# Kernel tuning notes

Measured on AMD Instinct MI355X. Metric: run time of the kernel, lower is better.

## Reference

```python
import jax, jax.numpy as jnp
import numpy as np

B, N1, N2, D, O = 4, 256, 256, 64, 64
TEMP = 1.0
BN_EPS = 1e-5


def setup_inputs() -> dict:
    key = jax.random.key(0)
    ks = jax.random.split(key, 24)
    s = lambda n: 1.0 / np.sqrt(n)
    inp = {
        'x1': jax.random.normal(ks[0], (B, N1, D), jnp.float32),
        'x2': jax.random.normal(ks[1], (B, N2, D), jnp.float32),
        'W_t1': jax.random.normal(ks[2], (D, D), jnp.float32) * s(D),
        'b_t1': jnp.zeros((D,), jnp.float32),
        'W_t2': jax.random.normal(ks[3], (D, D), jnp.float32) * s(D),
        'b_t2': jnp.zeros((D,), jnp.float32),
        'W_att': jax.random.normal(ks[4], (D, O), jnp.float32) * s(D),
        'b_att': jnp.zeros((O,), jnp.float32),
        'W_attM': jax.random.normal(ks[5], (D, O), jnp.float32) * s(D),
        'b_attM': jnp.zeros((O,), jnp.float32),
        'w11': jax.random.normal(ks[6], (O, 1), jnp.float32) * s(O),
        'w22': jax.random.normal(ks[7], (O, 1), jnp.float32) * s(O),
        'w12': jax.random.normal(ks[8], (O, 1), jnp.float32) * s(O),
        'wM': jax.random.normal(ks[9], (O, 1), jnp.float32) * s(O),
        'W_pa': jax.random.normal(ks[10], (D, O), jnp.float32) * s(D),
        'b_pa': jnp.zeros((O,), jnp.float32),
        'W_po': jax.random.normal(ks[11], (D, O), jnp.float32) * s(D),
        'b_po': jnp.zeros((O,), jnp.float32),
        'W_paM': jax.random.normal(ks[12], (D, O), jnp.float32) * s(D),
        'b_paM': jnp.zeros((O,), jnp.float32),
        'W_poM': jax.random.normal(ks[13], (D, O), jnp.float32) * s(D),
        'b_poM': jnp.zeros((O,), jnp.float32),
        'gamma': jnp.ones((O,), jnp.float32),
        'beta': jnp.zeros((O,), jnp.float32),
    }
    return inp


def _forward(x1, x2, W_t1, b_t1, W_t2, b_t2, W_att, b_att, W_attM, b_attM,
             w11, w22, w12, wM, W_pa, b_pa, W_po, b_po, W_paM, b_paM,
             W_poM, b_poM, gamma, beta):
    n1 = x1.shape[1]
    h1 = x1 @ W_t1 + b_t1                      # (B,n1,D)
    h2 = x2 @ W_t2 + b_t2                      # (B,n2,D)
    x = jnp.concatenate([h1, h2], axis=1)      # (B,N,D)
    master = jnp.mean(x, axis=1, keepdims=True)  # (B,1,D)

    # --- type-blocked attention map ---
    pair = x[:, :, None, :] * x[:, None, :, :]          # (B,N,N,D)
    e = jnp.tanh(pair @ W_att + b_att)                   # (B,N,N,O)
    s11 = jnp.einsum('bijd,d->bij', e[:, :n1, :n1], w11[:, 0])
    s12 = jnp.einsum('bijd,d->bij', e[:, :n1, n1:], w12[:, 0])
    s21 = jnp.einsum('bijd,d->bij', e[:, n1:, :n1], w12[:, 0])
    s22 = jnp.einsum('bijd,d->bij', e[:, n1:, n1:], w22[:, 0])
    top = jnp.concatenate([s11, s12], axis=2)
    bot = jnp.concatenate([s21, s22], axis=2)
    scores = jnp.concatenate([top, bot], axis=1)         # (B,N,N)
    att = jax.nn.softmax(scores / TEMP, axis=2)          # softmax over source nodes (torch dim=-2 of (B,N,N,1))

    # --- master update ---
    m = jnp.tanh((x * master) @ W_attM + b_attM)         # (B,N,O)
    aM = jax.nn.softmax((m @ wM) / TEMP, axis=1)         # (B,N,1)
    agg_m = jnp.einsum('bn,bnd->bd', aM[:, :, 0], x)[:, None, :]  # (B,1,D)
    master_new = (agg_m @ W_paM + b_paM) + (master @ W_poM + b_poM)

    # --- node projection + BN(eval) + SELU ---
    agg = jnp.einsum('bij,bjd->bid', att, x)             # (B,N,D)
    y = (agg @ W_pa + b_pa) + (x @ W_po + b_po)          # (B,N,O)
    y = y / jnp.sqrt(1.0 + BN_EPS) * gamma + beta        # BN eval: mean=0, var=1
    y = jax.nn.selu(y)
    return y[:, :n1], y[:, n1:], master_new


def reference(x1, x2, W_t1, b_t1, W_t2, b_t2, W_att, b_att, W_attM, b_attM,
              w11, w22, w12, wM, W_pa, b_pa, W_po, b_po, W_paM, b_paM,
              W_poM, b_poM, gamma, beta):
    return _forward(x1, x2, W_t1, b_t1, W_t2, b_t2, W_att, b_att, W_attM,
                    b_attM, w11, w22, w12, wM, W_pa, b_pa, W_po, b_po,
                    W_paM, b_paM, W_poM, b_poM, gamma, beta)
```

## Files before the change

kernel.cpp:

```cpp
#include <hip/hip_runtime.h>

#define BB 4
#define NN 512
#define NH 256
#define DD 64

typedef __attribute__((ext_vector_type(8))) short bf16x8;
typedef __attribute__((ext_vector_type(16))) float f32x16;
union BF8 { bf16x8 v; unsigned int u[4]; };

__device__ __forceinline__ float wred_sum(float v) {
  v += __shfl_xor(v, 32);
  v += __shfl_xor(v, 16);
  v += __shfl_xor(v, 8);
  v += __shfl_xor(v, 4);
  v += __shfl_xor(v, 2);
  v += __shfl_xor(v, 1);
  return v;
}

__device__ __forceinline__ float wred_max(float v) {
  v = fmaxf(v, __shfl_xor(v, 32));
  v = fmaxf(v, __shfl_xor(v, 16));
  v = fmaxf(v, __shfl_xor(v, 8));
  v = fmaxf(v, __shfl_xor(v, 4));
  v = fmaxf(v, __shfl_xor(v, 2));
  v = fmaxf(v, __shfl_xor(v, 1));
  return v;
}

__device__ __forceinline__ unsigned int cvtpk_bf16(float lo, float hi) {
  unsigned int r;
  asm("v_cvt_pk_bf16_f32 %0, %1, %2" : "=v"(r) : "v"(lo), "v"(hi));
  return r;
}

__device__ __forceinline__ float fast_exp2(float x) {
  float r;
  asm("v_exp_f32 %0, %1" : "=v"(r) : "v"(x));
  return r;
}

__device__ __forceinline__ float fast_tanh(float t) {
  t = fminf(15.f, fmaxf(-15.f, t));
  float z = __expf(2.f * t);
  return 1.f - 2.f * __builtin_amdgcn_rcpf(z + 1.f);
}

__device__ __forceinline__ float bflo(unsigned int u) { return __uint_as_float(u << 16); }
__device__ __forceinline__ float bfhi(unsigned int u) { return __uint_as_float(u & 0xffff0000u); }

__global__ __launch_bounds__(256)
void k1_build_x(const float* __restrict__ x1, const float* __restrict__ x2,
                const float* __restrict__ W_t1, const float* __restrict__ b_t1,
                const float* __restrict__ W_t2, const float* __restrict__ b_t2,
                float* __restrict__ X) {
  const int tid = threadIdx.x;
  const int lane = tid & 63;
  const int rq = tid >> 6;
  const int r = blockIdx.x * 4 + rq;
  const int b = r >> 9;
  const int n = r & 511;
  const float* src; const float* W; const float* bias;
  if (n < NH) { src = x1 + (b * NH + n) * DD;        W = W_t1; bias = b_t1; }
  else        { src = x2 + (b * NH + (n - NH)) * DD; W = W_t2; bias = b_t2; }
  const float4* s4 = reinterpret_cast<const float4*>(src);
  float t0 = 0.f, t1 = 0.f, t2 = 0.f, t3 = 0.f;
#pragma unroll
  for (int c = 0; c < 16; ++c) {
    const float4 v = s4[c];
    t0 = fmaf(v.x, W[(4 * c + 0) * DD + lane], t0);
    t1 = fmaf(v.y, W[(4 * c + 1) * DD + lane], t1);
    t2 = fmaf(v.z, W[(4 * c + 2) * DD + lane], t2);
    t3 = fmaf(v.w, W[(4 * c + 3) * DD + lane], t3);
  }
  X[r * DD + lane] = ((t0 + t1) + (t2 + t3)) + bias[lane];
}

__global__ __launch_bounds__(512, 1)
void k_sc(const float* __restrict__ X,
          const float* __restrict__ W_att, const float* __restrict__ b_att,
          const float* __restrict__ w11, const float* __restrict__ w22,
          const float* __restrict__ w12,
          float* __restrict__ scG) {
  const int b = blockIdx.y;
  const int bx = blockIdx.x;
  const int tid = threadIdx.x;
  const int lane = tid & 63;
  const int w = tid >> 6;
  const int l31 = lane & 31;
  const int half = lane >> 5;

  __shared__ __align__(16) float tblB[64];
  __shared__ __align__(16) float tblW[4][64];
  __shared__ __align__(16) float swv4[4];

  const float* __restrict__ Xb = X + b * NN * DD;
  float* __restrict__ scb = scG + b * NN * NN;
  const float K2E = 2.8853900817779268f;

  if (tid < 64) {
    const int ot = tid >> 5, hf = (tid >> 4) & 1, r = tid & 15;
    const int o = ot * 32 + (r & 3) + 8 * (r >> 2) + 4 * hf;
    tblB[tid] = K2E * b_att[o];
  }
  if (tid >= 64 && tid < 320) {
    const int t = tid - 64;
    const int comb = t >> 6;
    const int idx = t & 63;
    const int ot = idx >> 5, hf = (idx >> 4) & 1, r = idx & 15;
    const int o = ot * 32 + (r & 3) + 8 * (r >> 2) + 4 * hf;
    const int it_ = comb >> 1, jt_ = comb & 1;
    const float* wsl = it_ ? (jt_ ? w22 : w12) : (jt_ ? w12 : w11);
    tblW[comb][idx] = -2.f * wsl[o];
  }
  if (w < 4) {
    const int it_ = w >> 1, jt_ = w & 1;
    const float* wsl = it_ ? (jt_ ? w22 : w12) : (jt_ ? w12 : w11);
    const float s = wred_sum(wsl[lane]);
    if (lane == 0) swv4[w] = s;
  }

  BF8 Wp[2][4];
#pragma unroll
  for (int ot = 0; ot < 2; ++ot)
#pragma unroll
    for (int kt = 0; kt < 4; ++kt) {
      const int o = ot * 32 + l31;
#pragma unroll
      for (int p = 0; p < 4; ++p) {
        const int d0 = kt * 16 + half * 8 + 2 * p;
        Wp[ot][kt].u[p] = cvtpk_bf16(W_att[d0 * DD + o], W_att[(d0 + 1) * DD + o]);
      }
    }

  __syncthreads();

  const int cminA = bx >> 4;
  const int n32A = 16 - cminA;
  const int rB = 510 - 2 * bx;
  const int cminB = (255 - bx) >> 4;
  const int njobs = 2 * (n32A + (16 - cminB));

#pragma unroll 1
  for (int t = w; t < njobs; t += 8) {
    int row, c32;
    if (t < 2 * n32A) { row = 2 * bx + (t & 1); c32 = cminA + (t >> 1); }
    else { const int tp = t - 2 * n32A; row = rB + (tp & 1); c32 = cminB + (tp >> 1); }
    const int j0 = c32 * 32;
    const int comb = ((row >= NH) ? 2 : 0) | ((j0 >= NH) ? 1 : 0);

    BF8 Xi[4], Xj[4];
#pragma unroll
    for (int kt = 0; kt < 4; ++kt) {
      const float* bi = Xb + row * DD + kt * 16 + half * 8;
      const float4 a = *reinterpret_cast<const float4*>(bi);
      const float4 c = *reinterpret_cast<const float4*>(bi + 4);
      Xi[kt].u[0] = cvtpk_bf16(a.x, a.y);
      Xi[kt].u[1] = cvtpk_bf16(a.z, a.w);
      Xi[kt].u[2] = cvtpk_bf16(c.x, c.y);
      Xi[kt].u[3] = cvtpk_bf16(c.z, c.w);
      const float* bj = Xb + (j0 + l31) * DD + kt * 16 + half * 8;
      const float4 aj = *reinterpret_cast<const float4*>(bj);
      const float4 cj = *reinterpret_cast<const float4*>(bj + 4);
      Xj[kt].u[0] = cvtpk_bf16(aj.x, aj.y);
      Xj[kt].u[1] = cvtpk_bf16(aj.z, aj.w);
      Xj[kt].u[2] = cvtpk_bf16(cj.x, cj.y);
      Xj[kt].u[3] = cvtpk_bf16(cj.z, cj.w);
    }

    f32x16 C0 = {}, C1 = {};
#pragma unroll
    for (int kt = 0; kt < 4; ++kt) {
      BF8 Bi;
#pragma unroll
      for (int p = 0; p < 4; ++p)
        Bi.u[p] = cvtpk_bf16(bflo(Xi[kt].u[p]) * bflo(Xj[kt].u[p]),
                             bfhi(Xi[kt].u[p]) * bfhi(Xj[kt].u[p]));
      C0 = __builtin_amdgcn_mfma_f32_32x32x16_bf16(Wp[0][kt].v, Bi.v, C0, 0, 0, 0);
      C1 = __builtin_amdgcn_mfma_f32_32x32x16_bf16(Wp[1][kt].v, Bi.v, C1, 0, 0, 0);
    }

    float p = 0.f;
    const int base = half * 16;
#pragma unroll
    for (int r = 0; r < 16; ++r) {
      const float a0 = fmaf(C0[r], K2E, tblB[base + r]);
      const float e0 = fast_exp2(a0);
      p = fmaf(tblW[comb][base + r], __builtin_amdgcn_rcpf(e0 + 1.f), p);
      const float a1 = fmaf(C1[r], K2E, tblB[32 + base + r]);
      const float e1 = fast_exp2(a1);
      p = fmaf(tblW[comb][32 + base + r], __builtin_amdgcn_rcpf(e1 + 1.f), p);
    }
    p += __shfl_xor(p, 32);
    if (lane < 32) {
      const int j = j0 + l31;
      if (j >= row) {
        const float val = swv4[comb] + p;
        scb[row * NN + j] = val;
        if (j > row) scb[j * NN + row] = val;
      }
    }
  }
}

__global__ __launch_bounds__(1024, 4)
void k_rest(const float* __restrict__ X, const float* __restrict__ scG,
            const float* __restrict__ W_attM, const float* __restrict__ b_attM,
            const float* __restrict__ wM,
            const float* __restrict__ W_pa, const float* __restrict__ b_pa,
            const float* __restrict__ W_po, const float* __restrict__ b_po,
            const float* __restrict__ gamma, const float* __restrict__ beta,
            float* __restrict__ master, float* __restrict__ logits,
            float* __restrict__ out) {
  const int b = blockIdx.y;
  const int i0 = blockIdx.x * 8;
  const int tid = threadIdx.x;
  const int lane = tid & 63;
  const int w = tid >> 6;

  __shared__ __align__(16) float Xlds[NN * DD];
  __shared__ __align__(16) float scL[8 * NN];
  __shared__ __align__(16) float red2[16][DD];
  __shared__ __align__(16) float aggL[8][DD];
  __shared__ __align__(16) float mastL[64];

  const float* __restrict__ Xb = X + b * NN * DD;

  {
    const int c4 = (tid & 15) * 4;
    const int rh = tid >> 4;
#pragma unroll
    for (int it = 0; it < 8; ++it) {
      const int r = it * 64 + rh;
      *reinterpret_cast<float4*>(&Xlds[r * DD + c4]) =
          *reinterpret_cast<const float4*>(&Xb[r * DD + c4]);
    }
  }
  {
    const int r8 = tid >> 7;
    const int c = (tid & 127) * 4;
    *reinterpret_cast<float4*>(&scL[r8 * NN + c]) =
        *reinterpret_cast<const float4*>(&scG[(b * NN + i0 + r8) * NN + c]);
  }
  __syncthreads();

  {
    float s = 0.f;
    for (int r = w * 32; r < w * 32 + 32; ++r) s += Xlds[r * DD + lane];
    red2[w][lane] = s;
  }
  __syncthreads();
  if (w == 0) {
    float s = 0.f;
#pragma unroll
    for (int k = 0; k < 16; ++k) s += red2[k][lane];
    s *= (1.f / 512.f);
    mastL[lane] = s;
    if (blockIdx.x == 0) master[b * DD + lane] = s;
  }

  const int row = w & 7, part = w >> 3;
  const int irow = i0 + row;
  float v[8];
#pragma unroll
  for (int k = 0; k < 8; ++k) v[k] = scL[row * NN + lane + 64 * k];
  __syncthreads();
  float mx = fmaxf(fmaxf(fmaxf(v[0], v[1]), fmaxf(v[2], v[3])),
                   fmaxf(fmaxf(v[4], v[5]), fmaxf(v[6], v[7])));
  mx = wred_max(mx);
  float ssum = 0.f;
#pragma unroll
  for (int k = 0; k < 8; ++k) { v[k] = __expf(v[k] - mx); ssum += v[k]; }
  ssum = wred_sum(ssum);
  const float inv = __builtin_amdgcn_rcpf(ssum);
#pragma unroll
  for (int k = 0; k < 4; ++k) {
    const int kk = part * 4 + k;
    scL[row * NN + lane + 64 * kk] = v[kk] * inv;
  }

  float a0 = 0.f, a1 = 0.f, a2 = 0.f, a3 = 0.f;
  const float* scr = &scL[row * NN + part * 256];
  const int xof = part * 256 * DD;
  for (int jj = 0; jj < 64; ++jj) {
    const float4 at = *reinterpret_cast<const float4*>(&scr[jj * 4]);
    a0 = fmaf(at.x, Xlds[xof + (jj * 4 + 0) * DD + lane], a0);
    a1 = fmaf(at.y, Xlds[xof + (jj * 4 + 1) * DD + lane], a1);
    a2 = fmaf(at.z, Xlds[xof + (jj * 4 + 2) * DD + lane], a2);
    a3 = fmaf(at.w, Xlds[xof + (jj * 4 + 3) * DD + lane], a3);
  }
  red2[w][lane] = (a0 + a1) + (a2 + a3);
  __syncthreads();

  if (part == 0) {
    const float aggv = red2[w][lane] + red2[w + 8][lane];
    aggL[row][lane] = aggv;
    float y = b_pa[lane] + b_po[lane];
#pragma unroll 8
    for (int d = 0; d < DD; ++d) {
      y = fmaf(aggL[row][d], W_pa[d * DD + lane], y);
      y = fmaf(Xlds[irow * DD + d], W_po[d * DD + lane], y);
    }
    const float RSQ = 0.9999950000374997f;
    y = y * RSQ * gamma[lane] + beta[lane];
    const float SC_ = 1.0507009873554805f;
    const float AL = 1.6732632423543772f;
    y = (y > 0.f) ? (SC_ * y) : (SC_ * AL * (__expf(y) - 1.f));
    const int off = (irow < NH) ? ((b * NH + irow) * DD + lane)
                                : (BB * NH * DD + (b * NH + (irow - NH)) * DD + lane);
    out[off] = y;
  } else {
    float lg = b_attM[lane];
#pragma unroll 8
    for (int d = 0; d < DD; ++d)
      lg = fmaf(Xlds[irow * DD + d] * mastL[d], W_attM[d * DD + lane], lg);
    const float th = fast_tanh(lg);
    const float s = wred_sum(th * wM[lane]);
    if (lane == 0) logits[b * NN + irow] = s;
  }
}

__global__ __launch_bounds__(256)
void k4_master_new(const float* __restrict__ X, const float* __restrict__ master,
                   const float* __restrict__ logits,
                   const float* __restrict__ W_paM, const float* __restrict__ b_paM,
                   const float* __restrict__ W_poM, const float* __restrict__ b_poM,
                   float* __restrict__ out) {
  const int b = blockIdx.x;
  const int tid = threadIdx.x;
  const int lane = tid & 63;
  const int q = tid >> 6;
  __shared__ float red[4][DD];
  __shared__ float r4[4];
  __shared__ float aggm_s[DD];
  __shared__ float mrow_s[DD];
  const float* lg = logits + b * NN;
  const float v0 = lg[tid];
  const float v1 = lg[tid + 256];
  float mx = wred_max(fmaxf(v0, v1));
  if (lane == 0) r4[q] = mx;
  __syncthreads();
  mx = fmaxf(fmaxf(r4[0], r4[1]), fmaxf(r4[2], r4[3]));
  float es = __expf(v0 - mx) + __expf(v1 - mx);
  es = wred_sum(es);
  __syncthreads();
  if (lane == 0) r4[q] = es;
  __syncthreads();
  const float S = r4[0] + r4[1] + r4[2] + r4[3];
  const float invS = 1.f / S;

  float acc = 0.f;
  for (int nn = q * 128; nn < q * 128 + 128; ++nn) {
    const float a = __expf(lg[nn] - mx);
    acc = fmaf(a, X[(b * NN + nn) * DD + lane], acc);
  }
  red[q][lane] = acc;
  __syncthreads();
  if (q == 0) {
    aggm_s[lane] =
        (red[0][lane] + red[1][lane] + red[2][lane] + red[3][lane]) * invS;
    mrow_s[lane] = master[b * DD + lane];
  }
  __syncthreads();
  float p = 0.f;
  for (int d = q * 16; d < q * 16 + 16; ++d) {
    p = fmaf(aggm_s[d], W_paM[d * DD + lane], p);
    p = fmaf(mrow_s[d], W_poM[d * DD + lane], p);
  }
  __syncthreads();
  red[q][lane] = p;
  __syncthreads();
  if (q == 0) {
    out[2 * BB * NH * DD + b * DD + lane] =
        red[0][lane] + red[1][lane] + red[2][lane] + red[3][lane] +
        b_paM[lane] + b_poM[lane];
  }
}

extern "C" void kernel_launch(void* const* d_in, const int* in_sizes, int n_in,
                              void* d_out, int out_size, void* d_ws, size_t ws_size,
                              hipStream_t stream) {
  const float* x1    = (const float*)d_in[0];
  const float* x2    = (const float*)d_in[1];
  const float* W_t1  = (const float*)d_in[2];
  const float* b_t1  = (const float*)d_in[3];
  const float* W_t2  = (const float*)d_in[4];
  const float* b_t2  = (const float*)d_in[5];
  const float* W_att = (const float*)d_in[6];
  const float* b_att = (const float*)d_in[7];
  const float* W_attM = (const float*)d_in[8];
  const float* b_attM = (const float*)d_in[9];
  const float* w11   = (const float*)d_in[10];
  const float* w22   = (const float*)d_in[11];
  const float* w12   = (const float*)d_in[12];
  const float* wM    = (const float*)d_in[13];
  const float* W_pa  = (const float*)d_in[14];
  const float* b_pa  = (const float*)d_in[15];
  const float* W_po  = (const float*)d_in[16];
  const float* b_po  = (const float*)d_in[17];
  const float* W_paM = (const float*)d_in[18];
  const float* b_paM = (const float*)d_in[19];
  const float* W_poM = (const float*)d_in[20];
  const float* b_poM = (const float*)d_in[21];
  const float* gamma = (const float*)d_in[22];
  const float* beta  = (const float*)d_in[23];

  float* ws     = (float*)d_ws;
  float* X      = ws;
  float* master = ws + 131072;
  float* logits = ws + 131328;
  float* scG    = ws + 133376;
  float* out    = (float*)d_out;

  k1_build_x<<<512, 256, 0, stream>>>(x1, x2, W_t1, b_t1, W_t2, b_t2, X);
  k_sc<<<dim3(128, 4), 512, 0, stream>>>(X, W_att, b_att, w11, w22, w12, scG);
  k_rest<<<dim3(64, 4), 1024, 0, stream>>>(X, scG, W_attM, b_attM, wM,
                                           W_pa, b_pa, W_po, b_po, gamma, beta,
                                           master, logits, out);
  k4_master_new<<<4, 256, 0, stream>>>(X, master, logits, W_paM, b_paM, W_poM, b_poM, out);
}
```

Before: 56.41 us.

## Precompute bf16 X copy and reduce score weights via second MFMA

```diff
diff --git a/kernel.cpp b/kernel.cpp
--- a/kernel.cpp
+++ b/kernel.cpp
@@ -8,6 +8,7 @@
 typedef __attribute__((ext_vector_type(8))) short bf16x8;
 typedef __attribute__((ext_vector_type(16))) float f32x16;
 union BF8 { bf16x8 v; unsigned int u[4]; };
+union BF8Q { bf16x8 v; uint4 q; };
 
 __device__ __forceinline__ float wred_sum(float v) {
   v += __shfl_xor(v, 32);
@@ -54,7 +55,7 @@
 void k1_build_x(const float* __restrict__ x1, const float* __restrict__ x2,
                 const float* __restrict__ W_t1, const float* __restrict__ b_t1,
                 const float* __restrict__ W_t2, const float* __restrict__ b_t2,
-                float* __restrict__ X) {
+                float* __restrict__ X, unsigned int* __restrict__ XbfG) {
   const int tid = threadIdx.x;
   const int lane = tid & 63;
   const int rq = tid >> 6;
@@ -74,11 +75,14 @@
     t2 = fmaf(v.z, W[(4 * c + 2) * DD + lane], t2);
     t3 = fmaf(v.w, W[(4 * c + 3) * DD + lane], t3);
   }
-  X[r * DD + lane] = ((t0 + t1) + (t2 + t3)) + bias[lane];
+  const float yv = ((t0 + t1) + (t2 + t3)) + bias[lane];
+  X[r * DD + lane] = yv;
+  const float nb = __shfl_down(yv, 1);
+  if ((lane & 1) == 0) XbfG[r * 32 + (lane >> 1)] = cvtpk_bf16(yv, nb);
 }
 
 __global__ __launch_bounds__(512, 1)
-void k_sc(const float* __restrict__ X,
+void k_sc(const unsigned int* __restrict__ Xbf,
           const float* __restrict__ W_att, const float* __restrict__ b_att,
           const float* __restrict__ w11, const float* __restrict__ w22,
           const float* __restrict__ w12,
@@ -92,10 +96,9 @@
   const int half = lane >> 5;
 
   __shared__ __align__(16) float tblB[64];
-  __shared__ __align__(16) float tblW[4][64];
-  __shared__ __align__(16) float swv4[4];
-
-  const float* __restrict__ Xb = X + b * NN * DD;
+  __shared__ __align__(16) unsigned int A2L[4][32];
+
+  const unsigned int* __restrict__ Xb = Xbf + b * NN * 32;
   float* __restrict__ scb = scG + b * NN * NN;
   const float K2E = 2.8853900817779268f;
 
@@ -105,20 +108,18 @@
     tblB[tid] = K2E * b_att[o];
   }
   if (tid >= 64 && tid < 320) {
-    const int t = tid - 64;
-    const int comb = t >> 6;
-    const int idx = t & 63;
-    const int ot = idx >> 5, hf = (idx >> 4) & 1, r = idx & 15;
-    const int o = ot * 32 + (r & 3) + 8 * (r >> 2) + 4 * hf;
-    const int it_ = comb >> 1, jt_ = comb & 1;
-    const float* wsl = it_ ? (jt_ ? w22 : w12) : (jt_ ? w12 : w11);
-    tblW[comb][idx] = -2.f * wsl[o];
-  }
-  if (w < 4) {
-    const int it_ = w >> 1, jt_ = w & 1;
-    const float* wsl = it_ ? (jt_ ? w22 : w12) : (jt_ ? w12 : w11);
-    const float s = wred_sum(wsl[lane]);
-    if (lane == 0) swv4[w] = s;
+    const int tt = tid - 64;
+    const int comb = tt >> 6;
+    const int idx = tt & 63;
+    if (idx < 32) {
+      const int ot = (idx >> 4) & 1, kg = (idx >> 3) & 1, hf = (idx >> 2) & 1, pp = idx & 3;
+      const int it_ = comb >> 1, jt_ = comb & 1;
+      const float* wsl = it_ ? (jt_ ? w22 : w12) : (jt_ ? w12 : w11);
+      const int e0 = 2 * pp, e1 = 2 * pp + 1;
+      const int o0 = ot * 32 + kg * 16 + (e0 & 3) + 8 * (e0 >> 2) + 4 * hf;
+      const int o1 = ot * 32 + kg * 16 + (e1 & 3) + 8 * (e1 >> 2) + 4 * hf;
+      A2L[comb][idx] = cvtpk_bf16(wsl[o0], wsl[o1]);
+    }
   }
 
   BF8 Wp[2][4];
@@ -128,9 +129,9 @@
     for (int kt = 0; kt < 4; ++kt) {
       const int o = ot * 32 + l31;
 #pragma unroll
-      for (int p = 0; p < 4; ++p) {
-        const int d0 = kt * 16 + half * 8 + 2 * p;
-        Wp[ot][kt].u[p] = cvtpk_bf16(W_att[d0 * DD + o], W_att[(d0 + 1) * DD + o]);
+      for (int pp = 0; pp < 4; ++pp) {
+        const int d0 = kt * 16 + half * 8 + 2 * pp;
+        Wp[ot][kt].u[pp] = cvtpk_bf16(W_att[d0 * DD + o], W_att[(d0 + 1) * DD + o]);
       }
     }
 
@@ -143,62 +144,61 @@
   const int njobs = 2 * (n32A + (16 - cminB));
 
 #pragma unroll 1
-  for (int t = w; t < njobs; t += 8) {
+  for (int jb = w; jb < njobs; jb += 8) {
     int row, c32;
-    if (t < 2 * n32A) { row = 2 * bx + (t & 1); c32 = cminA + (t >> 1); }
-    else { const int tp = t - 2 * n32A; row = rB + (tp & 1); c32 = cminB + (tp >> 1); }
+    if (jb < 2 * n32A) { row = 2 * bx + (jb & 1); c32 = cminA + (jb >> 1); }
+    else { const int tp = jb - 2 * n32A; row = rB + (tp & 1); c32 = cminB + (tp >> 1); }
     const int j0 = c32 * 32;
     const int comb = ((row >= NH) ? 2 : 0) | ((j0 >= NH) ? 1 : 0);
 
-    BF8 Xi[4], Xj[4];
+    BF8 Bi[4];
 #pragma unroll
     for (int kt = 0; kt < 4; ++kt) {
-      const float* bi = Xb + row * DD + kt * 16 + half * 8;
-      const float4 a = *reinterpret_cast<const float4*>(bi);
-      const float4 c = *reinterpret_cast<const float4*>(bi + 4);
-      Xi[kt].u[0] = cvtpk_bf16(a.x, a.y);
-      Xi[kt].u[1] = cvtpk_bf16(a.z, a.w);
-      Xi[kt].u[2] = cvtpk_bf16(c.x, c.y);
-      Xi[kt].u[3] = cvtpk_bf16(c.z, c.w);
-      const float* bj = Xb + (j0 + l31) * DD + kt * 16 + half * 8;
-      const float4 aj = *reinterpret_cast<const float4*>(bj);
-      const float4 cj = *reinterpret_cast<const float4*>(bj + 4);
-      Xj[kt].u[0] = cvtpk_bf16(aj.x, aj.y);
-      Xj[kt].u[1] = cvtpk_bf16(aj.z, aj.w);
-      Xj[kt].u[2] = cvtpk_bf16(cj.x, cj.y);
-      Xj[kt].u[3] = cvtpk_bf16(cj.z, cj.w);
+      const uint4 xi = *reinterpret_cast<const uint4*>(Xb + row * 32 + kt * 8 + half * 4);
+      const uint4 xj = *reinterpret_cast<const uint4*>(Xb + (j0 + l31) * 32 + kt * 8 + half * 4);
+      Bi[kt].u[0] = cvtpk_bf16(bflo(xi.x) * bflo(xj.x), bfhi(xi.x) * bfhi(xj.x));
+      Bi[kt].u[1] = cvtpk_bf16(bflo(xi.y) * bflo(xj.y), bfhi(xi.y) * bfhi(xj.y));
+      Bi[kt].u[2] = cvtpk_bf16(bflo(xi.z) * bflo(xj.z), bfhi(xi.z) * bfhi(xj.z));
+      Bi[kt].u[3] = cvtpk_bf16(bflo(xi.w) * bflo(xj.w), bfhi(xi.w) * bfhi(xj.w));
     }
 
     f32x16 C0 = {}, C1 = {};
 #pragma unroll
     for (int kt = 0; kt < 4; ++kt) {
-      BF8 Bi;
-#pragma unroll
-      for (int p = 0; p < 4; ++p)
-        Bi.u[p] = cvtpk_bf16(bflo(Xi[kt].u[p]) * bflo(Xj[kt].u[p]),
-                             bfhi(Xi[kt].u[p]) * bfhi(Xj[kt].u[p]));
-      C0 = __builtin_amdgcn_mfma_f32_32x32x16_bf16(Wp[0][kt].v, Bi.v, C0, 0, 0, 0);
-      C1 = __builtin_amdgcn_mfma_f32_32x32x16_bf16(Wp[1][kt].v, Bi.v, C1, 0, 0, 0);
-    }
-
-    float p = 0.f;
+      C0 = __builtin_amdgcn_mfma_f32_32x32x16_bf16(Wp[0][kt].v, Bi[kt].v, C0, 0, 0, 0);
+      C1 = __builtin_amdgcn_mfma_f32_32x32x16_bf16(Wp[1][kt].v, Bi[kt].v, C1, 0, 0, 0);
+    }
+
+    f32x16 D2 = {};
     const int base = half * 16;
 #pragma unroll
-    for (int r = 0; r < 16; ++r) {
-      const float a0 = fmaf(C0[r], K2E, tblB[base + r]);
-      const float e0 = fast_exp2(a0);
-      p = fmaf(tblW[comb][base + r], __builtin_amdgcn_rcpf(e0 + 1.f), p);
-      const float a1 = fmaf(C1[r], K2E, tblB[32 + base + r]);
-      const float e1 = fast_exp2(a1);
-      p = fmaf(tblW[comb][32 + base + r], __builtin_amdgcn_rcpf(e1 + 1.f), p);
-    }
-    p += __shfl_xor(p, 32);
+    for (int ot = 0; ot < 2; ++ot) {
+      float tv[16];
+#pragma unroll
+      for (int r = 0; r < 16; ++r) {
+        const float Cr = (ot == 0) ? C0[r] : C1[r];
+        const float arg = fmaf(Cr, K2E, tblB[ot * 32 + base + r]);
+        const float e = fast_exp2(arg);
+        tv[r] = fmaf(-2.f, __builtin_amdgcn_rcpf(e + 1.f), 1.f);
+      }
+      BF8 B2a, B2b;
+#pragma unroll
+      for (int pp = 0; pp < 4; ++pp) {
+        B2a.u[pp] = cvtpk_bf16(tv[2 * pp], tv[2 * pp + 1]);
+        B2b.u[pp] = cvtpk_bf16(tv[8 + 2 * pp], tv[9 + 2 * pp]);
+      }
+      BF8Q A2a, A2b;
+      A2a.q = *reinterpret_cast<const uint4*>(&A2L[comb][ot * 16 + half * 4]);
+      A2b.q = *reinterpret_cast<const uint4*>(&A2L[comb][ot * 16 + 8 + half * 4]);
+      D2 = __builtin_amdgcn_mfma_f32_32x32x16_bf16(A2a.v, B2a.v, D2, 0, 0, 0);
+      D2 = __builtin_amdgcn_mfma_f32_32x32x16_bf16(A2b.v, B2b.v, D2, 0, 0, 0);
+    }
+    const float pout = D2[0];
     if (lane < 32) {
       const int j = j0 + l31;
       if (j >= row) {
-        const float val = swv4[comb] + p;
-        scb[row * NN + j] = val;
-        if (j > row) scb[j * NN + row] = val;
+        scb[row * NN + j] = pout;
+        if (j > row) scb[j * NN + row] = pout;
       }
     }
   }
@@ -411,10 +411,11 @@
   float* master = ws + 131072;
   float* logits = ws + 131328;
   float* scG    = ws + 133376;
+  unsigned int* Xbf = (unsigned int*)(ws + 133376 + 1048576);
   float* out    = (float*)d_out;
 
-  k1_build_x<<<512, 256, 0, stream>>>(x1, x2, W_t1, b_t1, W_t2, b_t2, X);
-  k_sc<<<dim3(128, 4), 512, 0, stream>>>(X, W_att, b_att, w11, w22, w12, scG);
+  k1_build_x<<<512, 256, 0, stream>>>(x1, x2, W_t1, b_t1, W_t2, b_t2, X, Xbf);
+  k_sc<<<dim3(128, 4), 512, 0, stream>>>(Xbf, W_att, b_att, w11, w22, w12, scG);
   k_rest<<<dim3(64, 4), 1024, 0, stream>>>(X, scG, W_attM, b_attM, wM,
                                            W_pa, b_pa, W_po, b_po, gamma, beta,
                                            master, logits, out);
```

Result: faster. 49.29 us (-12.6%).
